# Optimization experiments

Hardware: AMD Instinct MI355X
Metric: run time of the kernel (lower is better)

Reference implementation:

```python
import jax, jax.numpy as jnp
import numpy as np

N = 4096
IN_SIZE = 512
MLP_W = 16
HID = 512
MID = 64  # hardcoded tgc2 output size in the torch module
OUT = 128
BN_EPS = 1e-5


def setup_inputs() -> dict:
    key = jax.random.key(0)
    ks = jax.random.split(key, 24)
    adj = (jax.random.uniform(ks[0], (N, N)) < 0.05).astype(jnp.float32)
    xdeg = jax.random.uniform(ks[1], (N, N), dtype=jnp.float32)
    ydeg = jax.random.uniform(ks[2], (N, N), dtype=jnp.float32)
    u = lambda k, sh, fan: jax.random.uniform(k, sh, jnp.float32, -1.0, 1.0) / np.sqrt(fan)
    return {
        "adj": adj, "xdeg": xdeg, "ydeg": ydeg,
        # edge MLP: 3 -> MLP_W -> 2
        "mlp_w1": u(ks[3], (3, MLP_W), 3), "mlp_b1": jnp.zeros((MLP_W,), jnp.float32),
        "mlp_w2": u(ks[4], (MLP_W, 2), MLP_W), "mlp_b2": jnp.zeros((2,), jnp.float32),
        # positional linear: Linear(N, in_size) applied to eye(N) -> pe = W^T + b
        "pe_w": u(ks[5], (N, IN_SIZE), N), "pe_b": jnp.zeros((IN_SIZE,), jnp.float32),
        # GCN weights
        "gc1_w": u(ks[6], (IN_SIZE, HID), HID),
        "lin2_w": u(ks[7], (HID, MID), HID), "lin2_b": jnp.zeros((MID,), jnp.float32),
        "gc3_w": u(ks[8], (MID, OUT), OUT),
        # BatchNorm (eval mode: running stats)
        "bn1_g": jnp.ones((HID,), jnp.float32), "bn1_b": jnp.zeros((HID,), jnp.float32),
        "bn1_m": jnp.zeros((HID,), jnp.float32), "bn1_v": jnp.ones((HID,), jnp.float32),
        "bn2_g": jnp.ones((OUT,), jnp.float32), "bn2_b": jnp.zeros((OUT,), jnp.float32),
        "bn2_m": jnp.zeros((OUT,), jnp.float32), "bn2_v": jnp.ones((OUT,), jnp.float32),
    }


def reference(adj, xdeg, ydeg, mlp_w1, mlp_b1, mlp_w2, mlp_b2, pe_w, pe_b,
              gc1_w, lin2_w, lin2_b, gc3_w,
              bn1_g, bn1_b, bn1_m, bn1_v, bn2_g, bn2_b, bn2_m, bn2_v):
    # Edge MLP + softmax over [adj, xdeg, ydeg] features; torch only computes it
    # at nonzero adj entries then scatters into a dense mask. Since the mask is
    # multiplied by adj, computing densely and multiplying is exactly equivalent.
    feats = jnp.stack([adj, xdeg, ydeg], axis=-1)          # [N, N, 3]
    h = jax.nn.relu(jnp.einsum('nmf,fw->nmw', feats, mlp_w1) + mlp_b1)
    logits = jnp.einsum('nmw,wc->nmc', h, mlp_w2) + mlp_b2  # [N, N, 2]
    mask = jax.nn.softmax(logits, axis=-1)[..., 1]          # [N, N]
    a = adj * mask + jnp.eye(adj.shape[0], dtype=adj.dtype)

    # Degree normalization: A' = D_row^{-1/2} A D_col^{-1/2} (broadcast, no diag matmuls)
    rowsum = jnp.sum(a, axis=1)
    colsum = jnp.sum(a, axis=0)
    d_row = jnp.where(rowsum > 0, rowsum ** -0.5, 0.0)
    d_col = jnp.where(colsum > 0, colsum ** -0.5, 0.0)
    a = d_row[:, None] * a * d_col[None, :]

    # pe = Linear(eye(N)) = W^T + b (eval mode, dropout off)
    pe = pe_w + pe_b[None, :]                               # [N, IN_SIZE]

    h = a @ (pe @ gc1_w)                                    # GCN layer 1
    h = (h - bn1_m) * (bn1_g / jnp.sqrt(bn1_v + BN_EPS)) + bn1_b
    h = h @ lin2_w + lin2_b                                 # tgc2
    mid = h
    h = jax.nn.relu(h)
    h = a @ (h @ gc3_w)                                     # GCN layer 3
    out = (h - bn2_m) * (bn2_g / jnp.sqrt(bn2_v + BN_EPS)) + bn2_b
    return out, mid
```

## Files before the change

### kernel.cpp

```cpp
#include <hip/hip_runtime.h>
#include <hip/hip_bf16.h>

#define NN 4096
#define INS 512
#define HIDW 512
#define MIDW 64
#define OUTW 128
#define CAP 384
#define SEG 96
#define BN_EPS 1e-5f
#define CS_BLOCKS 256
#define CS_ROWS (NN / CS_BLOCKS)
#define NSTRIP 8
#define NPAIR (NSTRIP / 2)
#define SLOTCAP (NSTRIP * SEG)

__device__ __forceinline__ void thin_block(
    const float* __restrict__ A, const float* __restrict__ B,
    const float* __restrict__ abias, float* __restrict__ C, int K, int bb)
{
    __shared__ float As[64][36];
    __shared__ float Bs[64][64];
    const int t = threadIdx.x;
    const int bm = bb * 32;
    const int c2 = t & 31, rg = t >> 5;

    float acc[4][2] = {};
    for (int k0 = 0; k0 < K; k0 += 64) {
        #pragma unroll
        for (int l = 0; l < 8; ++l) {
            int e = t + l * 256;
            int r = e >> 6, k = e & 63;
            float v = A[(size_t)(bm + r) * K + k0 + k];
            if (abias) v += abias[k0 + k];
            As[k][r] = v;
        }
        #pragma unroll
        for (int l = 0; l < 16; ++l) {
            int e = t + l * 256;
            int k = e >> 6, n = e & 63;
            Bs[k][n] = B[(size_t)(k0 + k) * 64 + n];
        }
        __syncthreads();
        #pragma unroll
        for (int k = 0; k < 64; ++k) {
            float4 a4 = *reinterpret_cast<const float4*>(&As[k][rg * 4]);
            float2 b2 = *reinterpret_cast<const float2*>(&Bs[k][2 * c2]);
            acc[0][0] = fmaf(a4.x, b2.x, acc[0][0]);
            acc[0][1] = fmaf(a4.x, b2.y, acc[0][1]);
            acc[1][0] = fmaf(a4.y, b2.x, acc[1][0]);
            acc[1][1] = fmaf(a4.y, b2.y, acc[1][1]);
            acc[2][0] = fmaf(a4.z, b2.x, acc[2][0]);
            acc[2][1] = fmaf(a4.z, b2.y, acc[2][1]);
            acc[3][0] = fmaf(a4.w, b2.x, acc[3][0]);
            acc[3][1] = fmaf(a4.w, b2.y, acc[3][1]);
        }
        __syncthreads();
    }
    #pragma unroll
    for (int u = 0; u < 4; ++u) {
        int r = bm + rg * 4 + u;
        *reinterpret_cast<float2*>(&C[(size_t)r * 64 + 2 * c2]) =
            make_float2(acc[u][0], acc[u][1]);
    }
}

__global__ __launch_bounds__(256) void k_count_prep(
    const float* __restrict__ adj,
    int* __restrict__ cslot, int* __restrict__ cnt, int* __restrict__ dflag,
    const float* __restrict__ lin2_w, const float* __restrict__ lin2_b,
    const float* __restrict__ bn1_g, const float* __restrict__ bn1_b,
    const float* __restrict__ bn1_m, const float* __restrict__ bn1_v,
    const float* __restrict__ bn2_g, const float* __restrict__ bn2_b,
    const float* __restrict__ bn2_m, const float* __restrict__ bn2_v,
    float* __restrict__ Wp, float* __restrict__ c1,
    float* __restrict__ s2g, float* __restrict__ t2g)
{
    const int t = threadIdx.x;
    if (blockIdx.x == 0) {
        __shared__ float t1s[HIDW];
        for (int h = t; h < HIDW; h += 256) {
            float s1 = bn1_g[h] * rsqrtf(bn1_v[h] + BN_EPS);
            t1s[h] = bn1_b[h] - bn1_m[h] * s1;
            for (int m = 0; m < MIDW; ++m)
                Wp[(size_t)h * MIDW + m] = s1 * lin2_w[(size_t)h * MIDW + m];
        }
        __syncthreads();
        if (t < MIDW) {
            float acc = lin2_b[t];
            for (int h = 0; h < HIDW; ++h)
                acc = fmaf(t1s[h], lin2_w[(size_t)h * MIDW + t], acc);
            c1[t] = acc;
        } else if (t >= 64 && t < 64 + OUTW) {
            int j = t - 64;
            float s2 = bn2_g[j] * rsqrtf(bn2_v[j] + BN_EPS);
            s2g[j] = s2;
            t2g[j] = bn2_b[j] - bn2_m[j] * s2;
        }
        return;
    }
    const int wave = t >> 6, lane = t & 63;
    const int gw = (blockIdx.x - 1) * 4 + wave;
    const int i = gw >> 3, s = gw & 7;
    const int colbase = s * 512;
    const float* __restrict__ base = adj + (size_t)i * NN + colbase + 4 * lane;
    float4 a4a = *reinterpret_cast<const float4*>(base);
    float4 a4b = *reinterpret_cast<const float4*>(base + 256);
    const float av[8] = {a4a.x, a4a.y, a4a.z, a4a.w,
                         a4b.x, a4b.y, a4b.z, a4b.w};
    int* __restrict__ slot = cslot + (size_t)i * SLOTCAP + s * SEG;
    const unsigned long long lt = (1ULL << lane) - 1ULL;
    int run = 0;
    #pragma unroll
    for (int c = 0; c < 8; ++c) {
        int col = colbase + ((c < 4) ? (4 * lane + c) : (256 + 4 * lane + c - 4));
        bool diag = (col == i);
        bool act = (av[c] != 0.f) || diag;
        if (diag) dflag[i] = (av[c] != 0.f) ? 1 : 0;
        unsigned long long m = __ballot(act);
        if (act) {
            int pos = run + __popcll(m & lt);
            if (pos < SEG) slot[pos] = col;
        }
        run += __popcll(m);
    }
    if (lane == 0) cnt[gw] = (run < SEG) ? run : SEG;
}

__global__ __launch_bounds__(256) void k_fill_w2(
    const float* __restrict__ xdeg, const float* __restrict__ ydeg,
    const int* __restrict__ cslot, const int* __restrict__ cnt,
    const int* __restrict__ dflag,
    const float* __restrict__ w1, const float* __restrict__ b1,
    const float* __restrict__ w2, const float* __restrict__ b2,
    float* __restrict__ a_vals, int* __restrict__ a_cols,
    float* __restrict__ rs_part,
    const float* __restrict__ gc1_w, const float* __restrict__ Wp,
    float* __restrict__ W2)
{
    if (blockIdx.x < INS / 32) {
        thin_block(gc1_w, Wp, nullptr, W2, HIDW, blockIdx.x);
        return;
    }
    __shared__ float shb[16], sw1x[16], sw1y[16], sw2[32], sb2[2];
    const int t = threadIdx.x;
    const int wave = t >> 6, lane = t & 63;
    if (t < 16) {
        shb[t]  = b1[t] + w1[t];
        sw1x[t] = w1[16 + t];
        sw1y[t] = w1[32 + t];
    }
    if (t < 32) sw2[t] = w2[t];
    if (t < 2)  sb2[t] = b2[t];
    __syncthreads();

    const int q = __builtin_amdgcn_readfirstlane(
        (blockIdx.x - INS / 32) * 4 + wave);
    const int i = q >> 2;
    const int sp = (q & 3) * 2;
    const int* __restrict__ cb = cnt + i * NSTRIP;
    int wb = 0;
    #pragma unroll
    for (int ss = 0; ss < NSTRIP; ++ss) if (ss < sp) wb += cb[ss];
    const int n0 = cb[sp];
    const int ntot = n0 + cb[sp + 1];
    const int hasde = dflag[i];
    const int* __restrict__ slot = cslot + (size_t)i * SLOTCAP + sp * SEG;
    const float* __restrict__ xrow = xdeg + (size_t)i * NN;
    const float* __restrict__ yrow = ydeg + (size_t)i * NN;
    float* __restrict__ gv = a_vals + (size_t)i * CAP;
    int*   __restrict__ gc = a_cols + (size_t)i * CAP;

    float local = 0.f;
    for (int p = lane; p < ntot; p += 64) {
        int col = (p < n0) ? slot[p] : slot[SEG + p - n0];
        float x = xrow[col];
        float y = yrow[col];
        float l0 = sb2[0], l1 = sb2[1];
        #pragma unroll
        for (int w = 0; w < 16; ++w) {
            float hw = fmaf(x, sw1x[w], shb[w]);
            hw = fmaf(y, sw1y[w], hw);
            hw = fmaxf(hw, 0.f);
            l0 = fmaf(hw, sw2[2 * w],     l0);
            l1 = fmaf(hw, sw2[2 * w + 1], l1);
        }
        float v = 1.f / (1.f + __expf(l0 - l1));
        if (col == i) v = hasde ? (v + 1.f) : 1.f;
        int gp = wb + p;
        if (gp < CAP) { gc[gp] = col; gv[gp] = v; }
        local += v;
    }
    #pragma unroll
    for (int o = 32; o >= 1; o >>= 1)
        local += __shfl_down(local, o, 64);
    if (lane == 0) rs_part[q] = local;
}

__global__ __launch_bounds__(256) void k_colsum_g(
    const float* __restrict__ a_vals, const int* __restrict__ a_cols,
    const int* __restrict__ cnt, float* __restrict__ P,
    const float* __restrict__ pe_w, const float* __restrict__ pe_b,
    const float* __restrict__ W2, float* __restrict__ G)
{
    if (blockIdx.x < NN / 32) {
        thin_block(pe_w, W2, pe_b, G, INS, blockIdx.x);
        return;
    }
    __shared__ float ls[NN];
    const int t = threadIdx.x;
    const int b = blockIdx.x - NN / 32;
    for (int j = t; j < NN; j += 256) ls[j] = 0.f;
    __syncthreads();
    const int r0 = b * CS_ROWS;
    for (int r = r0; r < r0 + CS_ROWS; ++r) {
        int n = 0;
        #pragma unroll
        for (int ss = 0; ss < NSTRIP; ++ss) n += cnt[r * NSTRIP + ss];
        n = (n < CAP) ? n : CAP;
        const float* __restrict__ vr = a_vals + (size_t)r * CAP;
        const int*   __restrict__ cr = a_cols + (size_t)r * CAP;
        for (int p = t; p < n; p += 256)
            atomicAdd(&ls[cr[p]], vr[p]);
    }
    __syncthreads();
    for (int j = t; j < NN; j += 256)
        P[(size_t)b * NN + j] = ls[j];
}

__global__ __launch_bounds__(512) void k_scale(
    const float* __restrict__ rs_part, const float* __restrict__ P,
    float* __restrict__ d_row, float* __restrict__ d_col)
{
    int j = blockIdx.x * 512 + threadIdx.x;
    float r = 0.f;
    #pragma unroll
    for (int s = 0; s < NPAIR; ++s) r += rs_part[j * NPAIR + s];
    d_row[j] = (r > 0.f) ? 1.f / sqrtf(r) : 0.f;
    float c = 0.f;
    for (int b = 0; b < CS_BLOCKS; ++b)
        c += P[(size_t)b * NN + j];
    d_col[j] = (c > 0.f) ? 1.f / sqrtf(c) : 0.f;
}

template <bool WITH_MID>
__global__ __launch_bounds__(256) void k_spmm(
    const float* __restrict__ a_vals, const int* __restrict__ a_cols,
    const int* __restrict__ cnt, const float* __restrict__ X,
    const float* __restrict__ d_row, const float* __restrict__ d_col,
    const float* __restrict__ c1,
    const float* __restrict__ gc3, const float* __restrict__ s2g,
    const float* __restrict__ t2g,
    float* __restrict__ O1, float* __restrict__ O2)
{
    __shared__ float sv[2][CAP];
    __shared__ int   scl[2][CAP];
    __shared__ float sacc[4][64];
    const int t = threadIdx.x;
    const int wave = t >> 6, lane = t & 63;
    const int rb = wave >> 1, h = wave & 1;
    const int i = blockIdx.x * 2 + rb;
    int n = 0;
    #pragma unroll
    for (int ss = 0; ss < NSTRIP; ++ss) n += cnt[i * NSTRIP + ss];
    n = (n < CAP) ? n : CAP;
    const int n16 = (n + 15) & ~15;
    const float* __restrict__ vrow = a_vals + (size_t)i * CAP;
    const int*   __restrict__ crow = a_cols + (size_t)i * CAP;

    for (int p = h * 64 + lane; p < n16; p += 128) {
        bool ok = p < n;
        int c = ok ? crow[p] : 0;
        float v = ok ? vrow[p] : 0.f;
        if (WITH_MID) v *= d_col[c];
        sv[rb][p]  = v;
        scl[rb][p] = c;
    }
    __syncthreads();

    const int eh = lane >> 5;
    const int lc = lane & 31;
    const int Q  = n16 >> 1;
    const int Qh = Q >> 1;

    float a0 = 0.f, a1 = 0.f;
    for (int q = h * Qh; q < (h + 1) * Qh; q += 4) {
        #pragma unroll
        for (int j = 0; j < 4; ++j) {
            int p = 2 * (q + j) + eh;
            float v = sv[rb][p];
            int c = scl[rb][p];
            float2 x = *reinterpret_cast<const float2*>(X + (size_t)c * 64 + 2 * lc);
            a0 = fmaf(v, x.x, a0);
            a1 = fmaf(v, x.y, a1);
        }
    }
    a0 += __shfl_xor(a0, 32);
    a1 += __shfl_xor(a1, 32);
    if (lane < 32) { sacc[wave][2 * lc] = a0; sacc[wave][2 * lc + 1] = a1; }
    __syncthreads();

    if (WITH_MID) {
        if (h == 0 && lane < 32) {
            float s0 = sacc[wave][2 * lc]     + sacc[wave + 1][2 * lc];
            float s1 = sacc[wave][2 * lc + 1] + sacc[wave + 1][2 * lc + 1];
            float dr = d_row[i];
            float dc = d_col[i];
            float m0 = fmaf(s0, dr, c1[2 * lc]);
            float m1 = fmaf(s1, dr, c1[2 * lc + 1]);
            *reinterpret_cast<float2*>(O1 + (size_t)i * 64 + 2 * lc) =
                make_float2(m0, m1);
            *reinterpret_cast<float2*>(O2 + (size_t)i * 64 + 2 * lc) =
                make_float2(dc * fmaxf(m0, 0.f), dc * fmaxf(m1, 0.f));
        }
    } else {
        if (h == 0 && lane < 32) {
            float dr = d_row[i];
            float s0 = (sacc[wave][2 * lc]     + sacc[wave + 1][2 * lc])     * dr;
            float s1 = (sacc[wave][2 * lc + 1] + sacc[wave + 1][2 * lc + 1]) * dr;
            sacc[wave][2 * lc]     = s0;
            sacc[wave][2 * lc + 1] = s1;
        }
        __syncthreads();
        const int rb2 = t >> 7;
        const int j = t & 127;
        const float* __restrict__ srow = sacc[2 * rb2];
        float acc = 0.f;
        #pragma unroll 8
        for (int k = 0; k < 64; ++k)
            acc = fmaf(srow[k], gc3[k * 128 + j], acc);
        int orow = blockIdx.x * 2 + rb2;
        O1[(size_t)orow * 128 + j] = fmaf(acc, s2g[j], t2g[j]);
    }
}

extern "C" void kernel_launch(void* const* d_in, const int* in_sizes, int n_in,
                              void* d_out, int out_size, void* d_ws, size_t ws_size,
                              hipStream_t stream) {
    const float* adj    = (const float*)d_in[0];
    const float* xdeg   = (const float*)d_in[1];
    const float* ydeg   = (const float*)d_in[2];
    const float* mlp_w1 = (const float*)d_in[3];
    const float* mlp_b1 = (const float*)d_in[4];
    const float* mlp_w2 = (const float*)d_in[5];
    const float* mlp_b2 = (const float*)d_in[6];
    const float* pe_w   = (const float*)d_in[7];
    const float* pe_b   = (const float*)d_in[8];
    const float* gc1_w  = (const float*)d_in[9];
    const float* lin2_w = (const float*)d_in[10];
    const float* lin2_b = (const float*)d_in[11];
    const float* gc3_w  = (const float*)d_in[12];
    const float* bn1_g  = (const float*)d_in[13];
    const float* bn1_b  = (const float*)d_in[14];
    const float* bn1_m  = (const float*)d_in[15];
    const float* bn1_v  = (const float*)d_in[16];
    const float* bn2_g  = (const float*)d_in[17];
    const float* bn2_b  = (const float*)d_in[18];
    const float* bn2_m  = (const float*)d_in[19];
    const float* bn2_v  = (const float*)d_in[20];

    float* out = (float*)d_out;
    float* mid = out + (size_t)NN * OUTW;

    char* w = (char*)d_ws;
    float* a_vals = (float*)w;  w += (size_t)NN * CAP * 4;
    int*   a_cols = (int*)w;    w += (size_t)NN * CAP * 4;
    int*   cslot  = (int*)w;    w += (size_t)NN * SLOTCAP * 4;
    int*   cnt    = (int*)w;    w += (size_t)NN * NSTRIP * 4;
    int*   dflag  = (int*)w;    w += (size_t)NN * 4;
    float* rs_part= (float*)w;  w += (size_t)NN * NPAIR * 4;
    float* d_row  = (float*)w;  w += (size_t)NN * 4;
    float* d_col  = (float*)w;  w += (size_t)NN * 4;
    float* P      = (float*)w;  w += (size_t)CS_BLOCKS * NN * 4;
    float* Wp     = (float*)w;  w += (size_t)HIDW * MIDW * 4;
    float* W2     = (float*)w;  w += (size_t)INS * MIDW * 4;
    float* c1     = (float*)w;  w += 256;
    float* s2g    = (float*)w;  w += 512;
    float* t2g    = (float*)w;  w += 512;
    float* G      = (float*)w;  w += (size_t)NN * MIDW * 4;
    float* R      = (float*)w;  w += (size_t)NN * MIDW * 4;

    k_count_prep<<<NN * NSTRIP / 4 + 1, 256, 0, stream>>>(
        adj, cslot, cnt, dflag, lin2_w, lin2_b, bn1_g, bn1_b, bn1_m, bn1_v,
        bn2_g, bn2_b, bn2_m, bn2_v, Wp, c1, s2g, t2g);
    k_fill_w2<<<INS / 32 + NN * NPAIR / 4, 256, 0, stream>>>(
        xdeg, ydeg, cslot, cnt, dflag, mlp_w1, mlp_b1, mlp_w2, mlp_b2,
        a_vals, a_cols, rs_part, gc1_w, Wp, W2);
    k_colsum_g<<<NN / 32 + CS_BLOCKS, 256, 0, stream>>>(
        a_vals, a_cols, cnt, P, pe_w, pe_b, W2, G);
    k_scale<<<NN / 512, 512, 0, stream>>>(rs_part, P, d_row, d_col);
    k_spmm<true><<<NN / 2, 256, 0, stream>>>(
        a_vals, a_cols, cnt, G, d_row, d_col, c1,
        nullptr, nullptr, nullptr, mid, R);
    k_spmm<false><<<NN / 2, 256, 0, stream>>>(
        a_vals, a_cols, cnt, R, d_row, d_col, nullptr,
        gc3_w, s2g, t2g, out, nullptr);
}
```

Baseline: 129.7 us.

## Partition column-sum by column strip to shrink shared histogram and partials

The column-sum blocks now each handle one 512-column strip (matching the per-strip counts) over a 64-row chunk, with one wave per row, instead of a full 4096-entry shared histogram over 16 rows. This cuts shared memory per block, the cost of zeroing and writing out partials, and the partial-sum buffer that k_scale reduces over (64 instead of 256 rows of partials). It relies on column entries being stored in strip order within each row, and waves now scan row-strip segments that may be short, which leaves lanes idle.

```diff
diff --git a/kernel.cpp b/kernel.cpp
--- a/kernel.cpp
+++ b/kernel.cpp
@@ -9,11 +9,11 @@
 #define CAP 384
 #define SEG 96
 #define BN_EPS 1e-5f
-#define CS_BLOCKS 256
-#define CS_ROWS (NN / CS_BLOCKS)
 #define NSTRIP 8
 #define NPAIR (NSTRIP / 2)
 #define SLOTCAP (NSTRIP * SEG)
+#define CS_CHUNKS 64
+#define CS_RC (NN / CS_CHUNKS)
 
 __device__ __forceinline__ void thin_block(
     const float* __restrict__ A, const float* __restrict__ B,
@@ -207,25 +207,30 @@
         thin_block(pe_w, W2, pe_b, G, INS, blockIdx.x);
         return;
     }
-    __shared__ float ls[NN];
+    __shared__ float ls[512];
     const int t = threadIdx.x;
+    const int wave = t >> 6, lane = t & 63;
     const int b = blockIdx.x - NN / 32;
-    for (int j = t; j < NN; j += 256) ls[j] = 0.f;
+    const int chunk = b >> 3, s = b & 7;
+    for (int j = t; j < 512; j += 256) ls[j] = 0.f;
     __syncthreads();
-    const int r0 = b * CS_ROWS;
-    for (int r = r0; r < r0 + CS_ROWS; ++r) {
-        int n = 0;
-        #pragma unroll
-        for (int ss = 0; ss < NSTRIP; ++ss) n += cnt[r * NSTRIP + ss];
-        n = (n < CAP) ? n : CAP;
-        const float* __restrict__ vr = a_vals + (size_t)r * CAP;
-        const int*   __restrict__ cr = a_cols + (size_t)r * CAP;
-        for (int p = t; p < n; p += 256)
-            atomicAdd(&ls[cr[p]], vr[p]);
+    const int r0 = chunk * CS_RC;
+    for (int r = r0 + wave; r < r0 + CS_RC; r += 4) {
+        const int* __restrict__ cb = cnt + r * NSTRIP;
+        int wb = 0;
+        #pragma unroll
+        for (int ss = 0; ss < NSTRIP; ++ss) if (ss < s) wb += cb[ss];
+        int ns = cb[s];
+        if (wb >= CAP) ns = 0;
+        else if (wb + ns > CAP) ns = CAP - wb;
+        const float* __restrict__ vr = a_vals + (size_t)r * CAP + wb;
+        const int*   __restrict__ cr = a_cols + (size_t)r * CAP + wb;
+        for (int p = lane; p < ns; p += 64)
+            atomicAdd(&ls[cr[p] - s * 512], vr[p]);
     }
     __syncthreads();
-    for (int j = t; j < NN; j += 256)
-        P[(size_t)b * NN + j] = ls[j];
+    for (int j = t; j < 512; j += 256)
+        P[(size_t)chunk * NN + s * 512 + j] = ls[j];
 }
 
 __global__ __launch_bounds__(512) void k_scale(
@@ -238,7 +243,7 @@
     for (int s = 0; s < NPAIR; ++s) r += rs_part[j * NPAIR + s];
     d_row[j] = (r > 0.f) ? 1.f / sqrtf(r) : 0.f;
     float c = 0.f;
-    for (int b = 0; b < CS_BLOCKS; ++b)
+    for (int b = 0; b < CS_CHUNKS; ++b)
         c += P[(size_t)b * NN + j];
     d_col[j] = (c > 0.f) ? 1.f / sqrtf(c) : 0.f;
 }
@@ -371,7 +376,7 @@
     float* rs_part= (float*)w;  w += (size_t)NN * NPAIR * 4;
     float* d_row  = (float*)w;  w += (size_t)NN * 4;
     float* d_col  = (float*)w;  w += (size_t)NN * 4;
-    float* P      = (float*)w;  w += (size_t)CS_BLOCKS * NN * 4;
+    float* P      = (float*)w;  w += (size_t)CS_CHUNKS * NN * 4;
     float* Wp     = (float*)w;  w += (size_t)HIDW * MIDW * 4;
     float* W2     = (float*)w;  w += (size_t)INS * MIDW * 4;
     float* c1     = (float*)w;  w += 256;
@@ -386,7 +391,7 @@
     k_fill_w2<<<INS / 32 + NN * NPAIR / 4, 256, 0, stream>>>(
         xdeg, ydeg, cslot, cnt, dflag, mlp_w1, mlp_b1, mlp_w2, mlp_b2,
         a_vals, a_cols, rs_part, gc1_w, Wp, W2);
-    k_colsum_g<<<NN / 32 + CS_BLOCKS, 256, 0, stream>>>(
+    k_colsum_g<<<NN / 32 + CS_CHUNKS * NSTRIP, 256, 0, stream>>>(
         a_vals, a_cols, cnt, P, pe_w, pe_b, W2, G);
     k_scale<<<NN / 512, 512, 0, stream>>>(rs_part, P, d_row, d_col);
     k_spmm<true><<<NN / 2, 256, 0, stream>>>(
```

After: 126.9 us. 1.02x faster.
